# Performance work log

Measured on AMD Instinct MI355X. Metric: run time of the kernel, lower is better.

## Reference

```python
import jax, jax.numpy as jnp
import numpy as np

B, T, DIM = 2, 2048, 1024
H, HD = 16, 64          # num_heads, head_dim (DIM = H*HD)
SCALE = 0.12            # fixed attn_scale in the module
ROPE_BASE = 1024.0
EPS = 1e-6


def _rope_tables(seq_len, head_dim):
    half = head_dim // 2
    keep = head_dim // 4
    active = (1.0 / ROPE_BASE) ** jnp.linspace(0.0, 1.0, keep, dtype=jnp.float32)
    inv_freq = jnp.concatenate([active, jnp.zeros(half - keep, dtype=jnp.float32)])
    theta = jnp.arange(seq_len, dtype=jnp.float32)[:, None] * inv_freq[None, :]  # [T, half]
    return jnp.cos(theta), jnp.sin(theta)


def _rms_norm(x):
    # F.rms_norm without learned scale
    return x * jax.lax.rsqrt(jnp.mean(x * x, axis=-1, keepdims=True) + EPS)


def _apply_rope(x_bthd, cos, sin):
    # x_bthd: [B,T,H,HD]; cos/sin: [T, HD/2]
    xf = x_bthd.astype(jnp.float32)
    x1, x2 = jnp.split(xf, 2, axis=-1)
    c = cos[None, :, None, :]
    s = sin[None, :, None, :]
    y = jnp.concatenate([x1 * c + x2 * s, -x1 * s + x2 * c], axis=-1)
    return y.astype(x_bthd.dtype)


def setup_inputs() -> dict:
    key = jax.random.key(0)
    k1, k2, k3, k4 = jax.random.split(key, 4)
    x = jax.random.normal(k1, (B, T, DIM), dtype=jnp.float32)
    ve = jax.random.normal(k2, (B, T, DIM), dtype=jnp.float32)
    sa_lambdas = jax.random.uniform(k3, (2,), dtype=jnp.float32)
    # additive causal mask, as SDPA receives a float mask cast to q dtype
    causal = jnp.tril(jnp.ones((T, T), dtype=bool))
    attn_mask = jnp.where(causal, 0.0, -1e9).astype(jnp.float32)[None, None]
    # qkvo weights; scaled like a typical linear init (original zero-inits W_o,
    # here kept random so the output is non-trivial for kernel testing)
    qkvo_w = jax.random.normal(k4, (4, DIM, DIM), dtype=jnp.float32) * (DIM ** -0.5)
    return {"x": x, "ve": ve, "sa_lambdas": sa_lambdas, "attn_mask": attn_mask, "qkvo_w": qkvo_w}


def reference(x, ve, sa_lambdas, attn_mask, qkvo_w):
    b, t, _ = x.shape
    # fused QKV projection: qkvo_w[:3] is [3, DIM, DIM], F.linear -> x @ W.T
    qkv = jnp.einsum('btd,ked->btke', x, qkvo_w[:3])          # [B,T,3,DIM]
    q = _rms_norm(qkv[:, :, 0].reshape(b, t, H, HD))
    k = _rms_norm(qkv[:, :, 1].reshape(b, t, H, HD))
    v = _rms_norm(qkv[:, :, 2].reshape(b, t, H, HD))
    cos, sin = _rope_tables(t, HD)
    q = _apply_rope(q, cos, sin)
    k = _apply_rope(k, cos, sin)
    # value-embedding blend
    v = sa_lambdas[0] * v + sa_lambdas[1] * ve.reshape(b, t, H, HD)
    # attention with fixed scale and additive mask
    scores = jnp.einsum('bthd,bshd->bhts', q, k) * SCALE + attn_mask
    att = jax.nn.softmax(scores, axis=-1)
    y = jnp.einsum('bhts,bshd->bthd', att, v).reshape(b, t, DIM)
    return y @ qkvo_w[3].T
```

## Files before the change

kernel.cpp:

```cpp
#include <hip/hip_runtime.h>
#include <hip/hip_bf16.h>
#include <stdint.h>

#define T_SEQ 2048
#define DIMSZ 1024
#define NH    16
#define HDIM  64
#define NBATCH 2
#define KVB   64
#define ATT_SCALE 0.12f
#define QSCALE (0.12f * 1.4426950408889634f)

typedef __attribute__((ext_vector_type(8))) __bf16 bf16x8;
typedef __attribute__((ext_vector_type(8))) ushort u16x8;
typedef __attribute__((ext_vector_type(4))) float f32x4;

#define GLOAD_LDS16(gp, lp)                                                            \
  __builtin_amdgcn_global_load_lds((const __attribute__((address_space(1))) void*)(gp),\
                                   (__attribute__((address_space(3))) void*)(lp),      \
                                   16, 0, 0)

__device__ __forceinline__ ushort f2bf(float f) {
  union { float f; uint32_t u; } v; v.f = f;
  uint32_t u = v.u;
  uint32_t r = (u + 0x7FFFu + ((u >> 16) & 1u)) >> 16;
  return (ushort)r;
}

__device__ __forceinline__ float bf2f(ushort h) {
  union { float f; uint32_t u; } v;
  v.u = ((uint32_t)h) << 16;
  return v.f;
}

__device__ __forceinline__ uint32_t pk2(float a, float b) {
  union { __hip_bfloat162 h; uint32_t u; } cv;
  cv.h = __hip_bfloat162(__float2bfloat16(a), __float2bfloat16(b));
  return cv.u;
}

__global__ __launch_bounds__(256) void prep_k(const float* __restrict__ x,
                                              const float* __restrict__ w,
                                              ushort* __restrict__ Xb,
                                              ushort* __restrict__ Wb,
                                              float* __restrict__ ctab,
                                              float* __restrict__ stab) {
  int bid = blockIdx.x;
  int tid = threadIdx.x;
  if (bid < 4096) {
    int i = (bid * 256 + tid) * 4;
    float4 v = *(const float4*)(x + i);
    ushort4 o;
    o.x = f2bf(v.x); o.y = f2bf(v.y); o.z = f2bf(v.z); o.w = f2bf(v.w);
    *(ushort4*)(Xb + i) = o;
  } else if (bid < 8192) {
    int i = ((bid - 4096) * 256 + tid) * 4;
    float4 v = *(const float4*)(w + i);
    ushort4 o;
    o.x = f2bf(v.x); o.y = f2bf(v.y); o.z = f2bf(v.z); o.w = f2bf(v.w);
    *(ushort4*)(Wb + i) = o;
  } else {
    int idx = (bid - 8192) * 256 + tid;
    int j = idx & 31, t = idx >> 5;
    float c = 1.f, s = 0.f;
    if (j < 16) {
      float inv = powf(1024.0f, -(float)j / 15.0f);
      float th = (float)t * inv;
      c = cosf(th);
      s = sinf(th);
    }
    ctab[idx] = c;
    stab[idx] = s;
  }
}

#define BM 128
#define BN 128
#define BKS 64

__global__ __launch_bounds__(256) void gemm_qkvc_k(const ushort* __restrict__ A,
                                                   const ushort* __restrict__ Bt,
                                                   ushort* __restrict__ C) {
  const int K = DIMSZ, N = 3 * DIMSZ;
  __shared__ __align__(16) ushort As[BM * BKS];
  __shared__ __align__(16) ushort Bs[BN * BKS];
  int tid = threadIdx.x;
  int wave = tid >> 6, lane = tid & 63;
  int lr = lane & 15, lg = lane >> 4;
  int m0 = blockIdx.x * BM, n0 = blockIdx.y * BN;
  int wm = (wave >> 1) * 64, wn = (wave & 1) * 64;

  int srow = tid >> 3;
  int sel = (((tid & 7) ^ (srow & 7)) << 3);

  f32x4 acc[4][4];
  for (int m = 0; m < 4; ++m)
    for (int n = 0; n < 4; ++n)
      acc[m][n] = (f32x4){0.f, 0.f, 0.f, 0.f};

  for (int k0 = 0; k0 < K; k0 += BKS) {
#pragma unroll
    for (int it = 0; it < 4; ++it) {
      GLOAD_LDS16(A + (size_t)(m0 + it * 32 + srow) * K + k0 + sel, &As[(it * 256 + tid) * 8]);
      GLOAD_LDS16(Bt + (size_t)(n0 + it * 32 + srow) * K + k0 + sel, &Bs[(it * 256 + tid) * 8]);
    }
    __syncthreads();
#pragma unroll
    for (int kk = 0; kk < 2; ++kk) {
      int cA = (((kk * 4 + lg) ^ (lr & 7)) << 3);
      bf16x8 af[4], bf[4];
#pragma unroll
      for (int m = 0; m < 4; ++m)
        af[m] = *(const bf16x8*)&As[(wm + m * 16 + lr) * BKS + cA];
#pragma unroll
      for (int n = 0; n < 4; ++n)
        bf[n] = *(const bf16x8*)&Bs[(wn + n * 16 + lr) * BKS + cA];
#pragma unroll
      for (int m = 0; m < 4; ++m)
#pragma unroll
        for (int n = 0; n < 4; ++n)
          acc[m][n] = __builtin_amdgcn_mfma_f32_16x16x32_bf16(af[m], bf[n], acc[m][n], 0, 0, 0);
    }
    __syncthreads();
  }
#pragma unroll
  for (int m = 0; m < 4; ++m)
#pragma unroll
    for (int n = 0; n < 4; ++n)
#pragma unroll
      for (int r = 0; r < 4; ++r) {
        int row = m0 + wm + m * 16 + lg * 4 + r;
        int col = n0 + wn + n * 16 + lr;
        C[(size_t)row * N + col] = f2bf(acc[m][n][r]);
      }
}

__global__ __launch_bounds__(256) void qkv_post_k(const ushort* __restrict__ QKVb,
                                                  const float* __restrict__ ve,
                                                  const float* __restrict__ lam,
                                                  const float* __restrict__ ctab,
                                                  const float* __restrict__ stab,
                                                  ushort* __restrict__ Qb,
                                                  ushort* __restrict__ Kb,
                                                  ushort* __restrict__ Vt) {
  int idx = blockIdx.x * 4 + (threadIdx.x >> 6);
  int lane = threadIdx.x & 63;
  int h = idx & (NH - 1);
  int bt = idx >> 4;
  int t = bt & (T_SEQ - 1);
  int b = bt >> 11;

  const ushort* base = QKVb + (size_t)bt * 3072 + h * HDIM + lane;
  float qv = bf2f(base[0]);
  float kv = bf2f(base[1024]);
  float vv = bf2f(base[2048]);

  float sq = qv * qv, sk = kv * kv, sv = vv * vv;
#pragma unroll
  for (int off = 1; off < 64; off <<= 1) {
    sq += __shfl_xor(sq, off);
    sk += __shfl_xor(sk, off);
    sv += __shfl_xor(sv, off);
  }
  qv *= rsqrtf(sq * (1.0f / 64.0f) + 1e-6f);
  kv *= rsqrtf(sk * (1.0f / 64.0f) + 1e-6f);
  vv *= rsqrtf(sv * (1.0f / 64.0f) + 1e-6f);

  int j = lane & 31;
  float c = ctab[t * 32 + j];
  float s = stab[t * 32 + j];
  float qo = __shfl_xor(qv, 32);
  float ko = __shfl_xor(kv, 32);
  float q2 = (lane < 32) ? (qv * c + qo * s) : (qv * c - qo * s);
  float k2 = (lane < 32) ? (kv * c + ko * s) : (kv * c - ko * s);
  float v2 = lam[0] * vv + lam[1] * ve[(size_t)bt * DIMSZ + h * HDIM + lane];

  q2 *= QSCALE;

  int bh = b * NH + h;
  Qb[((size_t)bh * T_SEQ + t) * HDIM + lane] = f2bf(q2);
  Kb[((size_t)bh * T_SEQ + t) * HDIM + lane] = f2bf(k2);
  Vt[((size_t)bh * HDIM + lane) * T_SEQ + t] = f2bf(v2);
}

__global__ __launch_bounds__(256) void gemm_out_k(const ushort* __restrict__ A,
                                                  const ushort* __restrict__ Bt,
                                                  float* __restrict__ C) {
  const int K = DIMSZ, N = DIMSZ;
  __shared__ __align__(16) ushort As[64 * BKS];
  __shared__ __align__(16) ushort Bs[128 * BKS];
  int tid = threadIdx.x;
  int wave = tid >> 6, lane = tid & 63;
  int lr = lane & 15, lg = lane >> 4;
  int m0 = blockIdx.x * 64, n0 = blockIdx.y * 128;
  int wm = (wave >> 1) * 32, wn = (wave & 1) * 64;

  int srow = tid >> 3;
  int sel = (((tid & 7) ^ (srow & 7)) << 3);

  f32x4 acc[2][4];
#pragma unroll
  for (int m = 0; m < 2; ++m)
#pragma unroll
    for (int n = 0; n < 4; ++n)
      acc[m][n] = (f32x4){0.f, 0.f, 0.f, 0.f};

  for (int k0 = 0; k0 < K; k0 += BKS) {
#pragma unroll
    for (int it = 0; it < 2; ++it)
      GLOAD_LDS16(A + (size_t)(m0 + it * 32 + srow) * K + k0 + sel, &As[(it * 256 + tid) * 8]);
#pragma unroll
    for (int it = 0; it < 4; ++it)
      GLOAD_LDS16(Bt + (size_t)(n0 + it * 32 + srow) * K + k0 + sel, &Bs[(it * 256 + tid) * 8]);
    __syncthreads();
#pragma unroll
    for (int kk = 0; kk < 2; ++kk) {
      int cA = (((kk * 4 + lg) ^ (lr & 7)) << 3);
      bf16x8 af[2], bf[4];
#pragma unroll
      for (int m = 0; m < 2; ++m)
        af[m] = *(const bf16x8*)&As[(wm + m * 16 + lr) * BKS + cA];
#pragma unroll
      for (int n = 0; n < 4; ++n)
        bf[n] = *(const bf16x8*)&Bs[(wn + n * 16 + lr) * BKS + cA];
#pragma unroll
      for (int m = 0; m < 2; ++m)
#pragma unroll
        for (int n = 0; n < 4; ++n)
          acc[m][n] = __builtin_amdgcn_mfma_f32_16x16x32_bf16(af[m], bf[n], acc[m][n], 0, 0, 0);
    }
    __syncthreads();
  }
#pragma unroll
  for (int m = 0; m < 2; ++m)
#pragma unroll
    for (int n = 0; n < 4; ++n)
#pragma unroll
      for (int r = 0; r < 4; ++r) {
        int row = m0 + wm + m * 16 + lg * 4 + r;
        int col = n0 + wn + n * 16 + lr;
        C[(size_t)row * N + col] = acc[m][n][r];
      }
}

__global__ __launch_bounds__(256, 4) void attn_k(const ushort* __restrict__ Q,
                                                 const ushort* __restrict__ K,
                                                 const ushort* __restrict__ Vt,
                                                 ushort* __restrict__ Y) {
  int bh = blockIdx.x;
  int qb = 31 - blockIdx.y;
  int tid = threadIdx.x;
  int wid = tid >> 6, lane = tid & 63;
  int lr = lane & 15, lg = lane >> 4;
  int b = bh >> 4, h = bh & 15;

  int r0 = qb * 64 + wid * 16;
  int nkv = qb + 1;

  __shared__ __align__(16) ushort Kl[2][KVB * HDIM];
  __shared__ __align__(16) ushort Vl[2][KVB * HDIM];
  __shared__ __align__(16) ushort Plds[4][16][64];

  const ushort* Kbh = K + (size_t)bh * T_SEQ * HDIM;
  const ushort* Vbh = Vt + (size_t)bh * HDIM * T_SEQ;

  int sr = tid >> 3;
  int sel = (((tid & 7) ^ (sr & 7)) << 3);
  const ushort* ksrc0 = Kbh + (size_t)sr * HDIM + sel;
  const ushort* ksrc1 = Kbh + (size_t)(sr + 32) * HDIM + sel;
  const ushort* vsrc0 = Vbh + (size_t)sr * T_SEQ + sel;
  const ushort* vsrc1 = Vbh + (size_t)(sr + 32) * T_SEQ + sel;
  int ld0 = tid * 8, ld1 = tid * 8 + 2048;

  const ushort* Qbase = Q + ((size_t)bh * T_SEQ + r0) * HDIM;
  bf16x8 aq[2];
#pragma unroll
  for (int kk = 0; kk < 2; ++kk)
    aq[kk] = *(const bf16x8*)(Qbase + (size_t)lr * HDIM + kk * 32 + lg * 8);

  int fcol[2];
  fcol[0] = ((0 + lg) ^ (lr & 7)) << 3;
  fcol[1] = ((4 + lg) ^ (lr & 7)) << 3;

  f32x4 o[4];
#pragma unroll
  for (int n = 0; n < 4; ++n) o[n] = (f32x4){0.f, 0.f, 0.f, 0.f};
  float lrow = 0.f;

  GLOAD_LDS16(ksrc0, &Kl[0][ld0]);
  GLOAD_LDS16(ksrc1, &Kl[0][ld1]);
  GLOAD_LDS16(vsrc0, &Vl[0][ld0]);
  GLOAD_LDS16(vsrc1, &Vl[0][ld1]);
  __syncthreads();

  for (int kb = 0; kb < nkv; ++kb) {
    int cur = kb & 1;
    if (kb + 1 < nkv) {
      size_t ko = (size_t)(kb + 1) * KVB * HDIM;
      int vo = (kb + 1) * KVB;
      GLOAD_LDS16(ksrc0 + ko, &Kl[cur ^ 1][ld0]);
      GLOAD_LDS16(ksrc1 + ko, &Kl[cur ^ 1][ld1]);
      GLOAD_LDS16(vsrc0 + vo, &Vl[cur ^ 1][ld0]);
      GLOAD_LDS16(vsrc1 + vo, &Vl[cur ^ 1][ld1]);
    }
    const ushort* Kc = &Kl[cur][0];
    const ushort* Vc = &Vl[cur][0];
    f32x4 s[4];
#pragma unroll
    for (int n = 0; n < 4; ++n) {
      f32x4 a = (f32x4){0.f, 0.f, 0.f, 0.f};
      bf16x8 kf0 = *(const bf16x8*)&Kc[(n * 16 + lr) * HDIM + fcol[0]];
      a = __builtin_amdgcn_mfma_f32_16x16x32_bf16(kf0, aq[0], a, 0, 0, 0);
      bf16x8 kf1 = *(const bf16x8*)&Kc[(n * 16 + lr) * HDIM + fcol[1]];
      a = __builtin_amdgcn_mfma_f32_16x16x32_bf16(kf1, aq[1], a, 0, 0, 0);
      s[n] = a;
    }
    if (kb == nkv - 1) {
      int qrow = r0 + lr;
      int kb0 = kb * KVB + lg * 4;
#pragma unroll
      for (int n = 0; n < 4; ++n)
#pragma unroll
        for (int r = 0; r < 4; ++r)
          if (kb0 + n * 16 + r > qrow) s[n][r] = -1e30f;
    }
    float psum = 0.f;
#pragma unroll
    for (int n = 0; n < 4; ++n) {
      float p0 = exp2f(s[n][0]), p1 = exp2f(s[n][1]);
      float p2 = exp2f(s[n][2]), p3 = exp2f(s[n][3]);
      psum += (p0 + p1) + (p2 + p3);
      uint2 w;
      w.x = pk2(p0, p1);
      w.y = pk2(p2, p3);
      int pw = (((n * 2 + (lg >> 1)) ^ (lr & 7)) << 3) + ((lg & 1) << 2);
      *(uint2*)&Plds[wid][lr][pw] = w;
    }
    lrow += psum;
#pragma unroll
    for (int kk = 0; kk < 2; ++kk) {
      bf16x8 ap = *(const bf16x8*)&Plds[wid][lr][((kk * 4 + lg) ^ (lr & 7)) << 3];
#pragma unroll
      for (int n = 0; n < 4; ++n) {
        bf16x8 vf = *(const bf16x8*)&Vc[(n * 16 + lr) * HDIM + fcol[kk]];
        o[n] = __builtin_amdgcn_mfma_f32_16x16x32_bf16(vf, ap, o[n], 0, 0, 0);
      }
    }
    __syncthreads();
  }
  lrow += __shfl_xor(lrow, 16);
  lrow += __shfl_xor(lrow, 32);
  float inv = 1.0f / lrow;
  int row = r0 + lr;
#pragma unroll
  for (int n = 0; n < 4; ++n) {
    uint2 w;
    w.x = pk2(o[n][0] * inv, o[n][1] * inv);
    w.y = pk2(o[n][2] * inv, o[n][3] * inv);
    *(uint2*)&Y[((size_t)b * T_SEQ + row) * DIMSZ + h * HDIM + n * 16 + lg * 4] = w;
  }
}

extern "C" void kernel_launch(void* const* d_in, const int* in_sizes, int n_in,
                              void* d_out, int out_size, void* d_ws, size_t ws_size,
                              hipStream_t stream) {
  const float* x   = (const float*)d_in[0];
  const float* ve  = (const float*)d_in[1];
  const float* lam = (const float*)d_in[2];
  const float* w   = (const float*)d_in[4];
  float* out = (float*)d_out;

  char* ws = (char*)d_ws;
  const size_t NTOK = (size_t)NBATCH * T_SEQ;

  ushort* Xb   = (ushort*)(ws);
  ushort* Wb   = (ushort*)(ws + 8388608);
  ushort* QKVb = (ushort*)(ws + 16777216);
  ushort* Qb   = (ushort*)(ws + 41943040);
  ushort* Kb   = (ushort*)(ws + 50331648);
  ushort* Vt   = (ushort*)(ws + 58720256);
  ushort* Yb   = (ushort*)(ws + 67108864);
  float*  ctab = (float*)(ws + 75497472);
  float*  stab = (float*)(ws + 75759616);

  prep_k<<<8448, 256, 0, stream>>>(x, w, Xb, Wb, ctab, stab);

  gemm_qkvc_k<<<dim3(4096 / BM, 3072 / BN), 256, 0, stream>>>(Xb, Wb, QKVb);

  qkv_post_k<<<(int)(NTOK * NH / 4), 256, 0, stream>>>(QKVb, ve, lam, ctab, stab, Qb, Kb, Vt);

  attn_k<<<dim3(NBATCH * NH, 32), 256, 0, stream>>>(Qb, Kb, Vt, Yb);

  gemm_out_k<<<dim3(4096 / 64, 1024 / 128), 256, 0, stream>>>(Yb, Wb + 3ull * DIMSZ * DIMSZ, out);
}
```

Measured before the change: 127.9 us.

## Process two query tiles per attention block to reuse K/V loads

Each attention block now handles 128 query rows, split into two 16-row tiles per wave, instead of 64. Every K/V tile loaded into LDS is therefore used for twice as many query rows, and the grid is halved. The first tile skips the last KV block, and each tile gets its own causal mask. In exchange, register pressure rises and fewer blocks are available to fill the GPU.

```diff
diff --git a/kernel.cpp b/kernel.cpp
--- a/kernel.cpp
+++ b/kernel.cpp
@@ -248,14 +248,15 @@
                                                  const ushort* __restrict__ Vt,
                                                  ushort* __restrict__ Y) {
   int bh = blockIdx.x;
-  int qb = 31 - blockIdx.y;
+  int qb = 15 - blockIdx.y;
   int tid = threadIdx.x;
   int wid = tid >> 6, lane = tid & 63;
   int lr = lane & 15, lg = lane >> 4;
   int b = bh >> 4, h = bh & 15;
 
-  int r0 = qb * 64 + wid * 16;
-  int nkv = qb + 1;
+  int rA = qb * 128 + wid * 16;
+  int rB = rA + 64;
+  int nkv = 2 * qb + 2;
 
   __shared__ __align__(16) ushort Kl[2][KVB * HDIM];
   __shared__ __align__(16) ushort Vl[2][KVB * HDIM];
@@ -272,20 +273,26 @@
   const ushort* vsrc1 = Vbh + (size_t)(sr + 32) * T_SEQ + sel;
   int ld0 = tid * 8, ld1 = tid * 8 + 2048;
 
-  const ushort* Qbase = Q + ((size_t)bh * T_SEQ + r0) * HDIM;
-  bf16x8 aq[2];
-#pragma unroll
-  for (int kk = 0; kk < 2; ++kk)
-    aq[kk] = *(const bf16x8*)(Qbase + (size_t)lr * HDIM + kk * 32 + lg * 8);
+  const ushort* QbaseA = Q + ((size_t)bh * T_SEQ + rA) * HDIM;
+  const ushort* QbaseB = Q + ((size_t)bh * T_SEQ + rB) * HDIM;
+  bf16x8 aqA[2], aqB[2];
+#pragma unroll
+  for (int kk = 0; kk < 2; ++kk) {
+    aqA[kk] = *(const bf16x8*)(QbaseA + (size_t)lr * HDIM + kk * 32 + lg * 8);
+    aqB[kk] = *(const bf16x8*)(QbaseB + (size_t)lr * HDIM + kk * 32 + lg * 8);
+  }
 
   int fcol[2];
   fcol[0] = ((0 + lg) ^ (lr & 7)) << 3;
   fcol[1] = ((4 + lg) ^ (lr & 7)) << 3;
 
-  f32x4 o[4];
-#pragma unroll
-  for (int n = 0; n < 4; ++n) o[n] = (f32x4){0.f, 0.f, 0.f, 0.f};
-  float lrow = 0.f;
+  f32x4 oA[4], oB[4];
+#pragma unroll
+  for (int n = 0; n < 4; ++n) {
+    oA[n] = (f32x4){0.f, 0.f, 0.f, 0.f};
+    oB[n] = (f32x4){0.f, 0.f, 0.f, 0.f};
+  }
+  float lrowA = 0.f, lrowB = 0.f;
 
   GLOAD_LDS16(ksrc0, &Kl[0][ld0]);
   GLOAD_LDS16(ksrc1, &Kl[0][ld1]);
@@ -305,59 +312,103 @@
     }
     const ushort* Kc = &Kl[cur][0];
     const ushort* Vc = &Vl[cur][0];
-    f32x4 s[4];
+    bool doA = (kb <= 2 * qb);
+
+    f32x4 sA[4], sB[4];
 #pragma unroll
     for (int n = 0; n < 4; ++n) {
-      f32x4 a = (f32x4){0.f, 0.f, 0.f, 0.f};
-      bf16x8 kf0 = *(const bf16x8*)&Kc[(n * 16 + lr) * HDIM + fcol[0]];
-      a = __builtin_amdgcn_mfma_f32_16x16x32_bf16(kf0, aq[0], a, 0, 0, 0);
-      bf16x8 kf1 = *(const bf16x8*)&Kc[(n * 16 + lr) * HDIM + fcol[1]];
-      a = __builtin_amdgcn_mfma_f32_16x16x32_bf16(kf1, aq[1], a, 0, 0, 0);
-      s[n] = a;
+      sA[n] = (f32x4){0.f, 0.f, 0.f, 0.f};
+      sB[n] = (f32x4){0.f, 0.f, 0.f, 0.f};
+    }
+#pragma unroll
+    for (int kk = 0; kk < 2; ++kk)
+#pragma unroll
+      for (int n = 0; n < 4; ++n) {
+        bf16x8 kf = *(const bf16x8*)&Kc[(n * 16 + lr) * HDIM + fcol[kk]];
+        if (doA) sA[n] = __builtin_amdgcn_mfma_f32_16x16x32_bf16(kf, aqA[kk], sA[n], 0, 0, 0);
+        sB[n] = __builtin_amdgcn_mfma_f32_16x16x32_bf16(kf, aqB[kk], sB[n], 0, 0, 0);
+      }
+    if (kb == 2 * qb) {
+      int qrow = rA + lr;
+      int kb0 = kb * KVB + lg * 4;
+#pragma unroll
+      for (int n = 0; n < 4; ++n)
+#pragma unroll
+        for (int r = 0; r < 4; ++r)
+          if (kb0 + n * 16 + r > qrow) sA[n][r] = -1e30f;
     }
     if (kb == nkv - 1) {
-      int qrow = r0 + lr;
+      int qrow = rB + lr;
       int kb0 = kb * KVB + lg * 4;
 #pragma unroll
       for (int n = 0; n < 4; ++n)
 #pragma unroll
         for (int r = 0; r < 4; ++r)
-          if (kb0 + n * 16 + r > qrow) s[n][r] = -1e30f;
-    }
-    float psum = 0.f;
-#pragma unroll
-    for (int n = 0; n < 4; ++n) {
-      float p0 = exp2f(s[n][0]), p1 = exp2f(s[n][1]);
-      float p2 = exp2f(s[n][2]), p3 = exp2f(s[n][3]);
-      psum += (p0 + p1) + (p2 + p3);
-      uint2 w;
-      w.x = pk2(p0, p1);
-      w.y = pk2(p2, p3);
-      int pw = (((n * 2 + (lg >> 1)) ^ (lr & 7)) << 3) + ((lg & 1) << 2);
-      *(uint2*)&Plds[wid][lr][pw] = w;
-    }
-    lrow += psum;
-#pragma unroll
-    for (int kk = 0; kk < 2; ++kk) {
-      bf16x8 ap = *(const bf16x8*)&Plds[wid][lr][((kk * 4 + lg) ^ (lr & 7)) << 3];
+          if (kb0 + n * 16 + r > qrow) sB[n][r] = -1e30f;
+    }
+    bf16x8 apA[2], apB[2];
+    if (doA) {
+      float ps = 0.f;
+#pragma unroll
+      for (int n = 0; n < 4; ++n) {
+        float p0 = exp2f(sA[n][0]), p1 = exp2f(sA[n][1]);
+        float p2 = exp2f(sA[n][2]), p3 = exp2f(sA[n][3]);
+        ps += (p0 + p1) + (p2 + p3);
+        uint2 w;
+        w.x = pk2(p0, p1);
+        w.y = pk2(p2, p3);
+        int pw = (((n * 2 + (lg >> 1)) ^ (lr & 7)) << 3) + ((lg & 1) << 2);
+        *(uint2*)&Plds[wid][lr][pw] = w;
+      }
+      lrowA += ps;
+#pragma unroll
+      for (int kk = 0; kk < 2; ++kk)
+        apA[kk] = *(const bf16x8*)&Plds[wid][lr][((kk * 4 + lg) ^ (lr & 7)) << 3];
+    }
+    {
+      float ps = 0.f;
+#pragma unroll
+      for (int n = 0; n < 4; ++n) {
+        float p0 = exp2f(sB[n][0]), p1 = exp2f(sB[n][1]);
+        float p2 = exp2f(sB[n][2]), p3 = exp2f(sB[n][3]);
+        ps += (p0 + p1) + (p2 + p3);
+        uint2 w;
+        w.x = pk2(p0, p1);
+        w.y = pk2(p2, p3);
+        int pw = (((n * 2 + (lg >> 1)) ^ (lr & 7)) << 3) + ((lg & 1) << 2);
+        *(uint2*)&Plds[wid][lr][pw] = w;
+      }
+      lrowB += ps;
+#pragma unroll
+      for (int kk = 0; kk < 2; ++kk)
+        apB[kk] = *(const bf16x8*)&Plds[wid][lr][((kk * 4 + lg) ^ (lr & 7)) << 3];
+    }
+#pragma unroll
+    for (int kk = 0; kk < 2; ++kk)
 #pragma unroll
       for (int n = 0; n < 4; ++n) {
         bf16x8 vf = *(const bf16x8*)&Vc[(n * 16 + lr) * HDIM + fcol[kk]];
-        o[n] = __builtin_amdgcn_mfma_f32_16x16x32_bf16(vf, ap, o[n], 0, 0, 0);
-      }
-    }
+        if (doA) oA[n] = __builtin_amdgcn_mfma_f32_16x16x32_bf16(vf, apA[kk], oA[n], 0, 0, 0);
+        oB[n] = __builtin_amdgcn_mfma_f32_16x16x32_bf16(vf, apB[kk], oB[n], 0, 0, 0);
+      }
     __syncthreads();
   }
-  lrow += __shfl_xor(lrow, 16);
-  lrow += __shfl_xor(lrow, 32);
-  float inv = 1.0f / lrow;
-  int row = r0 + lr;
+  lrowA += __shfl_xor(lrowA, 16);
+  lrowA += __shfl_xor(lrowA, 32);
+  lrowB += __shfl_xor(lrowB, 16);
+  lrowB += __shfl_xor(lrowB, 32);
+  float invA = 1.0f / lrowA;
+  float invB = 1.0f / lrowB;
+  int rowA = rA + lr, rowB = rB + lr;
 #pragma unroll
   for (int n = 0; n < 4; ++n) {
-    uint2 w;
-    w.x = pk2(o[n][0] * inv, o[n][1] * inv);
-    w.y = pk2(o[n][2] * inv, o[n][3] * inv);
-    *(uint2*)&Y[((size_t)b * T_SEQ + row) * DIMSZ + h * HDIM + n * 16 + lg * 4] = w;
+    uint2 wa, wb;
+    wa.x = pk2(oA[n][0] * invA, oA[n][1] * invA);
+    wa.y = pk2(oA[n][2] * invA, oA[n][3] * invA);
+    wb.x = pk2(oB[n][0] * invB, oB[n][1] * invB);
+    wb.y = pk2(oB[n][2] * invB, oB[n][3] * invB);
+    *(uint2*)&Y[((size_t)b * T_SEQ + rowA) * DIMSZ + h * HDIM + n * 16 + lg * 4] = wa;
+    *(uint2*)&Y[((size_t)b * T_SEQ + rowB) * DIMSZ + h * HDIM + n * 16 + lg * 4] = wb;
   }
 }
 
@@ -389,7 +440,7 @@
 
   qkv_post_k<<<(int)(NTOK * NH / 4), 256, 0, stream>>>(QKVb, ve, lam, ctab, stab, Qb, Kb, Vt);
 
-  attn_k<<<dim3(NBATCH * NH, 32), 256, 0, stream>>>(Qb, Kb, Vt, Yb);
+  attn_k<<<dim3(NBATCH * NH, 16), 256, 0, stream>>>(Qb, Kb, Vt, Yb);
 
   gemm_out_k<<<dim3(4096 / 64, 1024 / 128), 256, 0, stream>>>(Yb, Wb + 3ull * DIMSZ * DIMSZ, out);
 }
```

Result: slower. 215.7 us (+68.6%).
